# Performance work log

Hardware: AMD Instinct MI355X
Metric: run time of the kernel (lower is better)

Reference implementation:

```python
import jax, jax.numpy as jnp
import numpy as np

N_HEADS = 4
D_HEAD = 32  # out_features // n_heads = 128 // 4
NEG_SLOPE = 0.2


def setup_inputs() -> dict:
    key = jax.random.key(0)
    k_x, k_adj, k_w, k_a = jax.random.split(key, 4)
    B, N, F_in, F_out = 4, 2048, 128, 128
    x = jax.random.normal(k_x, (B, N, F_in), dtype=jnp.float32)
    adj = jax.random.randint(k_adj, (B, N, N), 0, 2, dtype=jnp.int32)
    # Linear weight stored as [in, out] (torch stores [out, in]; math identical: x @ W)
    w_scale = np.sqrt(2.0 / (F_in + F_out))  # xavier-ish
    W = jax.random.normal(k_w, (F_in, F_out), dtype=jnp.float32) * w_scale
    a = jax.random.normal(k_a, (N_HEADS, 2 * D_HEAD), dtype=jnp.float32) * np.sqrt(2.0 / (2 * D_HEAD))
    return {"x": x, "adj": adj, "W": W, "a": a}


def reference(x, adj, W, a):
    B, N, _ = x.shape
    # project and split heads: [B, H, N, D]
    h = jnp.einsum('bnf,fo->bno', x, W).reshape(B, N, N_HEADS, D_HEAD).transpose(0, 2, 1, 3)
    # additive attention logits
    e_src = jnp.einsum('bhnd,hd->bhn', h, a[:, :D_HEAD])  # [B,H,N]
    e_dst = jnp.einsum('bhnd,hd->bhn', h, a[:, D_HEAD:])  # [B,H,N]
    e = e_src[:, :, :, None] + e_dst[:, :, None, :]       # [B,H,N,N]
    e = jnp.where(e > 0, e, NEG_SLOPE * e)                # leaky_relu(0.2)
    mask = (adj[:, None, :, :] == 0)                      # [B,1,N,N] -> broadcast over heads
    e = jnp.where(mask, -jnp.inf, e)
    alpha = jax.nn.softmax(e, axis=-1)                    # dropout omitted (eval mode)
    out = jnp.einsum('bhnm,bhmd->bhnd', alpha, h)         # weighted aggregation
    out = out.transpose(0, 2, 1, 3).reshape(B, N, N_HEADS * D_HEAD)
    return jax.nn.elu(out)
```

## Files before the change

kernel.cpp:

```cpp
#include <hip/hip_runtime.h>
#include <hip/hip_bf16.h>

#define BB 4
#define NN 2048
#define FIN 128
#define NH 4
#define DH 32
#define NS 0.2f

typedef unsigned int u32;
typedef unsigned short u16;
typedef unsigned long long u64;
typedef __attribute__((ext_vector_type(8))) short short8;
typedef __attribute__((ext_vector_type(4))) float f32x4;
typedef __attribute__((ext_vector_type(4))) unsigned int u32x4;

#define OFF_ES 0
#define OFF_PQ 65536
#define OFF_HT 131088
#define OFF_BITS 655376

__device__ __forceinline__ u16 f2bf_rne(float f) {
  unsigned u = __float_as_uint(f);
  return (u16)((u + 0x7fffu + ((u >> 16) & 1u)) >> 16);
}

__device__ __forceinline__ int bitmask(u32 w, int e) {
#if __has_builtin(__builtin_amdgcn_sbfe)
  return __builtin_amdgcn_sbfe((int)w, e, 1);
#else
  return ((int)(w << (31 - e))) >> 31;
#endif
}

__global__ __launch_bounds__(256) void k_pack(const int* __restrict__ adj,
                                              u32* __restrict__ bits) {
  const int row = (blockIdx.x << 2) | (threadIdx.x >> 6);
  const int lane = threadIdx.x & 63;
  const int* src = adj + (size_t)row * NN;
  u32* dst = bits + (size_t)row * 64;
#pragma unroll 8
  for (int it = 0; it < 32; ++it) {
    const int v = src[it * 64 + lane];
    const u64 m = __ballot(v != 0);
    if (lane == 0) *(u64*)(dst + it * 2) = m;
  }
}

__global__ __launch_bounds__(256) void k_proj(
    const float* __restrict__ x, const float* __restrict__ W,
    const float* __restrict__ a, u16* __restrict__ hT,
    float* __restrict__ e_src, u32* __restrict__ PQ) {
  __shared__ float Ws[FIN * 128];
  const int tid = threadIdx.x;
  const int f = tid & 127, g = tid >> 7;
  const float4* Wg4 = (const float4*)W;
  float4* Ws4 = (float4*)Ws;
#pragma unroll
  for (int t = 0; t < 16; ++t) Ws4[t * 256 + tid] = Wg4[t * 256 + tid];
  __syncthreads();

  const int rb = blockIdx.x * 16 + g * 8;
  const int head = f >> 5, d = f & 31;
  const int b = rb >> 11, n0 = rb & (NN - 1);
  const int bh = b * NH + head;
  const float a_s = a[head * (2 * DH) + d];
  const float a_d = a[head * (2 * DH) + DH + d];

  float acc[8];
#pragma unroll
  for (int r = 0; r < 8; ++r) acc[r] = 0.f;

  const float* xb = x + (size_t)rb * FIN;
  for (int k = 0; k < FIN; ++k) {
    const float wv = Ws[k * 128 + f];
#pragma unroll
    for (int r = 0; r < 8; ++r) acc[r] = fmaf(wv, xb[r * FIN + k], acc[r]);
  }

  u16 hs[8];
#pragma unroll
  for (int r = 0; r < 8; ++r) hs[r] = f2bf_rne(acc[r]);
  u16* dst = hT + ((size_t)bh * DH + d) * NN + n0;
  *(int4*)dst = *(int4*)&hs[0];

#pragma unroll
  for (int r = 0; r < 8; ++r) {
    float s1 = acc[r] * a_s;
    float s2 = acc[r] * a_d;
#pragma unroll
    for (int off = 16; off >= 1; off >>= 1) {
      s1 += __shfl_xor(s1, off);
      s2 += __shfl_xor(s2, off);
    }
    if (d == 0) {
      e_src[(size_t)bh * NN + n0 + r] = s1;
      const u32 pb = f2bf_rne(__expf(s2));
      const u32 qb = f2bf_rne(__expf(NS * s2));
      PQ[(size_t)bh * NN + n0 + r] = (qb << 16) | pb;
    }
  }
}

__global__ __launch_bounds__(256, 4) void k_attn(
    const u16* __restrict__ hT, const float* __restrict__ e_src,
    const u32* __restrict__ PQv, const u32* __restrict__ bits,
    float* __restrict__ out) {
  __shared__ __align__(16) u16 smem[4][2][32 * 64];

  const int bid = blockIdx.x;
  const int bh = bid >> 6;
  const int it = bid & 63;
  const int b = bh >> 2, head = bh & 3;

  const int w = threadIdx.x >> 6;
  const int lane = threadIdx.x & 63;
  const int lg = lane >> 4, lm = lane & 15;

  const int i0 = it * 32 + lm;
  const int i1 = i0 + 16;
  const float es0 = e_src[(size_t)bh * NN + i0];
  const float es1 = e_src[(size_t)bh * NN + i1];
  const float A0 = __expf(es0), B0 = __expf(NS * es0);
  const float A1 = __expf(es1), B1 = __expf(NS * es1);

  const u32* PQb = PQv + (size_t)bh * NN + w * 512;
  const u16* hb = hT + (size_t)bh * DH * NN + w * 512;
  const u32* br0 = bits + ((size_t)b * NN + i0) * 64 + w * 16;
  const u32* br1 = bits + ((size_t)b * NN + i1) * 64 + w * 16;
  const int shamt = lg * 8;
  const int jb = lg * 8;

  u32 wd0[16], wd1[16];
#pragma unroll
  for (int q = 0; q < 4; ++q) {
    const u32x4 v0 = *(const u32x4*)(br0 + q * 4);
    const u32x4 v1 = *(const u32x4*)(br1 + q * 4);
#pragma unroll
    for (int k2 = 0; k2 < 4; ++k2) { wd0[q * 4 + k2] = v0[k2]; wd1[q * 4 + k2] = v1[k2]; }
  }

  const int sd = lane >> 3;
  const int sj = (lane & 7) * 8;
  u16* stg0 = &smem[w][0][0];
  u16* stg1 = &smem[w][1][0];
  const int woff = (sd * 64 + sj) ^ (sd << 3);

  short8 ones;
#pragma unroll
  for (int e = 0; e < 8; ++e) ones[e] = (short)0x3F80;

  f32x4 acc00 = {0,0,0,0}, acc01 = {0,0,0,0};
  f32x4 acc10 = {0,0,0,0}, acc11 = {0,0,0,0};
  f32x4 accS0 = {0,0,0,0}, accS1 = {0,0,0,0};

  {
    int4 r0 = *(const int4*)(hb + (size_t)(0 * 8 + sd) * NN + sj);
    int4 r1 = *(const int4*)(hb + (size_t)(1 * 8 + sd) * NN + sj);
    int4 r2 = *(const int4*)(hb + (size_t)(2 * 8 + sd) * NN + sj);
    int4 r3 = *(const int4*)(hb + (size_t)(3 * 8 + sd) * NN + sj);
    *(int4*)(stg0 + woff) = r0;
    *(int4*)(stg0 + woff + 1 * 512) = r1;
    *(int4*)(stg0 + woff + 2 * 512) = r2;
    *(int4*)(stg0 + woff + 3 * 512) = r3;
  }

  const int ra0 = (lm * 64) ^ ((lm & 7) << 3);

#pragma unroll
  for (int s = 0; s < 8; ++s) {
    u16* cur = (s & 1) ? stg1 : stg0;
    u16* nxt = (s & 1) ? stg0 : stg1;
    int4 n0, n1, n2, n3;
    if (s < 7) {
      const u16* g = hb + (s + 1) * 64;
      n0 = *(const int4*)(g + (size_t)(0 * 8 + sd) * NN + sj);
      n1 = *(const int4*)(g + (size_t)(1 * 8 + sd) * NN + sj);
      n2 = *(const int4*)(g + (size_t)(2 * 8 + sd) * NN + sj);
      n3 = *(const int4*)(g + (size_t)(3 * 8 + sd) * NN + sj);
    }
#pragma unroll
    for (int c = 0; c < 2; ++c) {
      const int jl = c * 32 + jb;
      const u32x4 pqa = *(const u32x4*)(PQb + s * 64 + jl);
      const u32x4 pqb = *(const u32x4*)(PQb + s * 64 + jl + 4);
      const short8 hv0 = *(const short8*)(cur + (ra0 ^ jl));
      const short8 hv1 = *(const short8*)(cur + ((ra0 ^ jl) + 16 * 64));
      const u32 wsh0 = wd0[s * 2 + c] >> shamt;
      const u32 wsh1 = wd1[s * 2 + c] >> shamt;
      short8 af0, af1;
#pragma unroll
      for (int e = 0; e < 8; ++e) {
        const u32 pq = (e < 4) ? pqa[e] : pqb[e - 4];
        const float Pf = __uint_as_float(pq << 16);
        const float Qf = __uint_as_float(pq & 0xffff0000u);
        const int m0 = bitmask(wsh0, e);
        const int m1 = bitmask(wsh1, e);
        float w0 = fmaxf(A0 * Pf, B0 * Qf);
        w0 = __int_as_float(__float_as_int(w0) & m0);
        af0[e] = (short)__builtin_bit_cast(unsigned short, __float2bfloat16(w0));
        float w1 = fmaxf(A1 * Pf, B1 * Qf);
        w1 = __int_as_float(__float_as_int(w1) & m1);
        af1[e] = (short)__builtin_bit_cast(unsigned short, __float2bfloat16(w1));
      }
      __builtin_amdgcn_s_setprio(1);
      acc00 = __builtin_amdgcn_mfma_f32_16x16x32_bf16(af0, hv0, acc00, 0, 0, 0);
      acc01 = __builtin_amdgcn_mfma_f32_16x16x32_bf16(af0, hv1, acc01, 0, 0, 0);
      acc10 = __builtin_amdgcn_mfma_f32_16x16x32_bf16(af1, hv0, acc10, 0, 0, 0);
      acc11 = __builtin_amdgcn_mfma_f32_16x16x32_bf16(af1, hv1, acc11, 0, 0, 0);
      accS0 = __builtin_amdgcn_mfma_f32_16x16x32_bf16(af0, ones, accS0, 0, 0, 0);
      accS1 = __builtin_amdgcn_mfma_f32_16x16x32_bf16(af1, ones, accS1, 0, 0, 0);
      __builtin_amdgcn_s_setprio(0);
    }
    if (s < 7) {
      *(int4*)(nxt + woff) = n0;
      *(int4*)(nxt + woff + 1 * 512) = n1;
      *(int4*)(nxt + woff + 2 * 512) = n2;
      *(int4*)(nxt + woff + 3 * 512) = n3;
    }
  }

  __syncthreads();
  float (*part)[32][33] = (float (*)[32][33]) & smem[0][0][0];
  float (*sp)[2][16] = (float (*)[2][16])((char*)&smem[0][0][0] + 16896);

#pragma unroll
  for (int r = 0; r < 4; ++r) {
    const int rl = lg * 4 + r;
    part[w][rl][lm] = acc00[r];
    part[w][rl][16 + lm] = acc01[r];
    part[w][16 + rl][lm] = acc10[r];
    part[w][16 + rl][16 + lm] = acc11[r];
  }
  if (lm == 0) {
#pragma unroll
    for (int r = 0; r < 4; ++r) {
      sp[w][0][lg * 4 + r] = accS0[r];
      sp[w][1][lg * 4 + r] = accS1[r];
    }
  }
  __syncthreads();

  const int tid = threadIdx.x;
#pragma unroll
  for (int t = 0; t < 4; ++t) {
    const int idx = t * 256 + tid;
    const int row = idx >> 5, d = idx & 31;
    const float v = part[0][row][d] + part[1][row][d] +
                    part[2][row][d] + part[3][row][d];
    const float s = sp[0][row >> 4][row & 15] + sp[1][row >> 4][row & 15] +
                    sp[2][row >> 4][row & 15] + sp[3][row >> 4][row & 15];
    const float o = v / s;
    const int n = it * 32 + row;
    out[((size_t)b * NN + n) * 128 + head * 32 + d] =
        o > 0.f ? o : (__expf(o) - 1.f);
  }
}

extern "C" void kernel_launch(void* const* d_in, const int* in_sizes, int n_in,
                              void* d_out, int out_size, void* d_ws, size_t ws_size,
                              hipStream_t stream) {
  const float* x = (const float*)d_in[0];
  const int* adj = (const int*)d_in[1];
  const float* W = (const float*)d_in[2];
  const float* a = (const float*)d_in[3];
  float* out = (float*)d_out;
  float* ws = (float*)d_ws;

  float* e_src = ws + OFF_ES;
  u32* PQv = (u32*)(ws + OFF_PQ);
  u16* hT = (u16*)(ws + OFF_HT);
  u32* bits = (u32*)(ws + OFF_BITS);

  k_pack<<<(BB * NN) / 4, 256, 0, stream>>>(adj, bits);
  k_proj<<<(BB * NN) / 16, 256, 0, stream>>>(x, W, a, hT, e_src, PQv);
  k_attn<<<BB * NH * 64, 256, 0, stream>>>(hT, e_src, PQv, bits, out);
}
```

Before: 62.67 us.

## Split attention key dimension across blocks and add combine kernel

Splits the neighbor (j) dimension of the attention kernel into two halves handled by separate blocks, writing unnormalized partial sums and softmax denominators to workspace, then adds a combine kernel that sums partials, normalizes and applies ELU. It also drops the LDS double-buffered staging of h and reads h fragments directly from global memory. The aim is more blocks for occupancy and shorter per-block work. In exchange it adds an extra kernel launch and round trip of partials through global memory, and uncoalesced direct global loads of h.

```diff
diff --git a/kernel.cpp b/kernel.cpp
--- a/kernel.cpp
+++ b/kernel.cpp
@@ -7,6 +7,7 @@
 #define NH 4
 #define DH 32
 #define NS 0.2f
+#define JP 2
 
 typedef unsigned int u32;
 typedef unsigned short u16;
@@ -15,10 +16,14 @@
 typedef __attribute__((ext_vector_type(4))) float f32x4;
 typedef __attribute__((ext_vector_type(4))) unsigned int u32x4;
 
-#define OFF_ES 0
-#define OFF_PQ 65536
-#define OFF_HT 131088
-#define OFF_BITS 655376
+#define OFF_ES   0
+#define OFF_PQ   32768
+#define OFF_HT   65536
+#define OFF_BITS 589824
+#define OFF_PACC 1114112
+#define OFF_PS   3211264
+#define PACC_STRIDE ((size_t)16 * NN * 32)
+#define PS_STRIDE   ((size_t)16 * NN)
 
 __device__ __forceinline__ u16 f2bf_rne(float f) {
   unsigned u = __float_as_uint(f);
@@ -102,16 +107,18 @@
   }
 }
 
-__global__ __launch_bounds__(256, 4) void k_attn(
+__global__ __launch_bounds__(256) void k_attn(
     const u16* __restrict__ hT, const float* __restrict__ e_src,
     const u32* __restrict__ PQv, const u32* __restrict__ bits,
-    float* __restrict__ out) {
-  __shared__ __align__(16) u16 smem[4][2][32 * 64];
+    float* __restrict__ pacc, float* __restrict__ pS) {
+  __shared__ float part[4][32][33];
+  __shared__ float sp[4][2][16];
 
   const int bid = blockIdx.x;
-  const int bh = bid >> 6;
+  const int jp = bid >> 10;
+  const int bh = (bid >> 6) & 15;
   const int it = bid & 63;
-  const int b = bh >> 2, head = bh & 3;
+  const int b = bh >> 2;
 
   const int w = threadIdx.x >> 6;
   const int lane = threadIdx.x & 63;
@@ -124,27 +131,24 @@
   const float A0 = __expf(es0), B0 = __expf(NS * es0);
   const float A1 = __expf(es1), B1 = __expf(NS * es1);
 
-  const u32* PQb = PQv + (size_t)bh * NN + w * 512;
-  const u16* hb = hT + (size_t)bh * DH * NN + w * 512;
-  const u32* br0 = bits + ((size_t)b * NN + i0) * 64 + w * 16;
-  const u32* br1 = bits + ((size_t)b * NN + i1) * 64 + w * 16;
+  const int jwbase = jp * 1024 + w * 256;
+  const u32* PQb = PQv + (size_t)bh * NN + jwbase;
+  const u16* hb0 = hT + ((size_t)bh * DH + lm) * NN + jwbase;
+  const u16* hb1 = hT + ((size_t)bh * DH + 16 + lm) * NN + jwbase;
+  const int wbase = jwbase >> 5;
+  const u32* br0 = bits + ((size_t)b * NN + i0) * 64 + wbase;
+  const u32* br1 = bits + ((size_t)b * NN + i1) * 64 + wbase;
   const int shamt = lg * 8;
   const int jb = lg * 8;
 
-  u32 wd0[16], wd1[16];
-#pragma unroll
-  for (int q = 0; q < 4; ++q) {
+  u32 wd0[8], wd1[8];
+#pragma unroll
+  for (int q = 0; q < 2; ++q) {
     const u32x4 v0 = *(const u32x4*)(br0 + q * 4);
     const u32x4 v1 = *(const u32x4*)(br1 + q * 4);
 #pragma unroll
     for (int k2 = 0; k2 < 4; ++k2) { wd0[q * 4 + k2] = v0[k2]; wd1[q * 4 + k2] = v1[k2]; }
   }
-
-  const int sd = lane >> 3;
-  const int sj = (lane & 7) * 8;
-  u16* stg0 = &smem[w][0][0];
-  u16* stg1 = &smem[w][1][0];
-  const int woff = (sd * 64 + sj) ^ (sd << 3);
 
   short8 ones;
 #pragma unroll
@@ -154,75 +158,39 @@
   f32x4 acc10 = {0,0,0,0}, acc11 = {0,0,0,0};
   f32x4 accS0 = {0,0,0,0}, accS1 = {0,0,0,0};
 
-  {
-    int4 r0 = *(const int4*)(hb + (size_t)(0 * 8 + sd) * NN + sj);
-    int4 r1 = *(const int4*)(hb + (size_t)(1 * 8 + sd) * NN + sj);
-    int4 r2 = *(const int4*)(hb + (size_t)(2 * 8 + sd) * NN + sj);
-    int4 r3 = *(const int4*)(hb + (size_t)(3 * 8 + sd) * NN + sj);
-    *(int4*)(stg0 + woff) = r0;
-    *(int4*)(stg0 + woff + 1 * 512) = r1;
-    *(int4*)(stg0 + woff + 2 * 512) = r2;
-    *(int4*)(stg0 + woff + 3 * 512) = r3;
-  }
-
-  const int ra0 = (lm * 64) ^ ((lm & 7) << 3);
-
-#pragma unroll
-  for (int s = 0; s < 8; ++s) {
-    u16* cur = (s & 1) ? stg1 : stg0;
-    u16* nxt = (s & 1) ? stg0 : stg1;
-    int4 n0, n1, n2, n3;
-    if (s < 7) {
-      const u16* g = hb + (s + 1) * 64;
-      n0 = *(const int4*)(g + (size_t)(0 * 8 + sd) * NN + sj);
-      n1 = *(const int4*)(g + (size_t)(1 * 8 + sd) * NN + sj);
-      n2 = *(const int4*)(g + (size_t)(2 * 8 + sd) * NN + sj);
-      n3 = *(const int4*)(g + (size_t)(3 * 8 + sd) * NN + sj);
-    }
-#pragma unroll
-    for (int c = 0; c < 2; ++c) {
-      const int jl = c * 32 + jb;
-      const u32x4 pqa = *(const u32x4*)(PQb + s * 64 + jl);
-      const u32x4 pqb = *(const u32x4*)(PQb + s * 64 + jl + 4);
-      const short8 hv0 = *(const short8*)(cur + (ra0 ^ jl));
-      const short8 hv1 = *(const short8*)(cur + ((ra0 ^ jl) + 16 * 64));
-      const u32 wsh0 = wd0[s * 2 + c] >> shamt;
-      const u32 wsh1 = wd1[s * 2 + c] >> shamt;
-      short8 af0, af1;
-#pragma unroll
-      for (int e = 0; e < 8; ++e) {
-        const u32 pq = (e < 4) ? pqa[e] : pqb[e - 4];
-        const float Pf = __uint_as_float(pq << 16);
-        const float Qf = __uint_as_float(pq & 0xffff0000u);
-        const int m0 = bitmask(wsh0, e);
-        const int m1 = bitmask(wsh1, e);
-        float w0 = fmaxf(A0 * Pf, B0 * Qf);
-        w0 = __int_as_float(__float_as_int(w0) & m0);
-        af0[e] = (short)__builtin_bit_cast(unsigned short, __float2bfloat16(w0));
-        float w1 = fmaxf(A1 * Pf, B1 * Qf);
-        w1 = __int_as_float(__float_as_int(w1) & m1);
-        af1[e] = (short)__builtin_bit_cast(unsigned short, __float2bfloat16(w1));
-      }
-      __builtin_amdgcn_s_setprio(1);
-      acc00 = __builtin_amdgcn_mfma_f32_16x16x32_bf16(af0, hv0, acc00, 0, 0, 0);
-      acc01 = __builtin_amdgcn_mfma_f32_16x16x32_bf16(af0, hv1, acc01, 0, 0, 0);
-      acc10 = __builtin_amdgcn_mfma_f32_16x16x32_bf16(af1, hv0, acc10, 0, 0, 0);
-      acc11 = __builtin_amdgcn_mfma_f32_16x16x32_bf16(af1, hv1, acc11, 0, 0, 0);
-      accS0 = __builtin_amdgcn_mfma_f32_16x16x32_bf16(af0, ones, accS0, 0, 0, 0);
-      accS1 = __builtin_amdgcn_mfma_f32_16x16x32_bf16(af1, ones, accS1, 0, 0, 0);
-      __builtin_amdgcn_s_setprio(0);
-    }
-    if (s < 7) {
-      *(int4*)(nxt + woff) = n0;
-      *(int4*)(nxt + woff + 1 * 512) = n1;
-      *(int4*)(nxt + woff + 2 * 512) = n2;
-      *(int4*)(nxt + woff + 3 * 512) = n3;
-    }
-  }
-
-  __syncthreads();
-  float (*part)[32][33] = (float (*)[32][33]) & smem[0][0][0];
-  float (*sp)[2][16] = (float (*)[2][16])((char*)&smem[0][0][0] + 16896);
+#pragma unroll
+  for (int t = 0; t < 8; ++t) {
+    const int jj = t * 32 + jb;
+    const u32x4 pqa = *(const u32x4*)(PQb + jj);
+    const u32x4 pqb = *(const u32x4*)(PQb + jj + 4);
+    const short8 hv0 = *(const short8*)(hb0 + jj);
+    const short8 hv1 = *(const short8*)(hb1 + jj);
+    const u32 wsh0 = wd0[t] >> shamt;
+    const u32 wsh1 = wd1[t] >> shamt;
+    short8 af0, af1;
+#pragma unroll
+    for (int e = 0; e < 8; ++e) {
+      const u32 pq = (e < 4) ? pqa[e] : pqb[e - 4];
+      const float Pf = __uint_as_float(pq << 16);
+      const float Qf = __uint_as_float(pq & 0xffff0000u);
+      const int m0 = bitmask(wsh0, e);
+      const int m1 = bitmask(wsh1, e);
+      float w0 = fmaxf(A0 * Pf, B0 * Qf);
+      w0 = __int_as_float(__float_as_int(w0) & m0);
+      af0[e] = (short)__builtin_bit_cast(unsigned short, __float2bfloat16(w0));
+      float w1 = fmaxf(A1 * Pf, B1 * Qf);
+      w1 = __int_as_float(__float_as_int(w1) & m1);
+      af1[e] = (short)__builtin_bit_cast(unsigned short, __float2bfloat16(w1));
+    }
+    __builtin_amdgcn_s_setprio(1);
+    acc00 = __builtin_amdgcn_mfma_f32_16x16x32_bf16(af0, hv0, acc00, 0, 0, 0);
+    acc01 = __builtin_amdgcn_mfma_f32_16x16x32_bf16(af0, hv1, acc01, 0, 0, 0);
+    acc10 = __builtin_amdgcn_mfma_f32_16x16x32_bf16(af1, hv0, acc10, 0, 0, 0);
+    acc11 = __builtin_amdgcn_mfma_f32_16x16x32_bf16(af1, hv1, acc11, 0, 0, 0);
+    accS0 = __builtin_amdgcn_mfma_f32_16x16x32_bf16(af0, ones, accS0, 0, 0, 0);
+    accS1 = __builtin_amdgcn_mfma_f32_16x16x32_bf16(af1, ones, accS1, 0, 0, 0);
+    __builtin_amdgcn_s_setprio(0);
+  }
 
 #pragma unroll
   for (int r = 0; r < 4; ++r) {
@@ -241,6 +209,8 @@
   }
   __syncthreads();
 
+  float* pa = pacc + ((size_t)jp * 16 + bh) * NN * 32;
+  float* ps = pS + ((size_t)jp * 16 + bh) * NN;
   const int tid = threadIdx.x;
 #pragma unroll
   for (int t = 0; t < 4; ++t) {
@@ -248,13 +218,34 @@
     const int row = idx >> 5, d = idx & 31;
     const float v = part[0][row][d] + part[1][row][d] +
                     part[2][row][d] + part[3][row][d];
-    const float s = sp[0][row >> 4][row & 15] + sp[1][row >> 4][row & 15] +
-                    sp[2][row >> 4][row & 15] + sp[3][row >> 4][row & 15];
-    const float o = v / s;
-    const int n = it * 32 + row;
-    out[((size_t)b * NN + n) * 128 + head * 32 + d] =
-        o > 0.f ? o : (__expf(o) - 1.f);
-  }
+    pa[(size_t)(it * 32 + row) * 32 + d] = v;
+    if (d == 0) {
+      const float s = sp[0][row >> 4][row & 15] + sp[1][row >> 4][row & 15] +
+                      sp[2][row >> 4][row & 15] + sp[3][row >> 4][row & 15];
+      ps[it * 32 + row] = s;
+    }
+  }
+}
+
+__global__ __launch_bounds__(256) void k_comb(
+    const float* __restrict__ pacc, const float* __restrict__ pS,
+    float* __restrict__ out) {
+  const int idx = blockIdx.x * 256 + threadIdx.x;
+  const int f = idx & 127;
+  const int g = idx >> 7;
+  const int b = g >> 11, n = g & (NN - 1);
+  const int head = f >> 5, d = f & 31;
+  const int bh = b * NH + head;
+  const size_t base = ((size_t)bh * NN + n) * 32 + d;
+  const size_t sbase = (size_t)bh * NN + n;
+  float v = 0.f, s = 0.f;
+#pragma unroll
+  for (int p = 0; p < JP; ++p) {
+    v += pacc[(size_t)p * PACC_STRIDE + base];
+    s += pS[(size_t)p * PS_STRIDE + sbase];
+  }
+  const float o = v / s;
+  out[idx] = o > 0.f ? o : (__expf(o) - 1.f);
 }
 
 extern "C" void kernel_launch(void* const* d_in, const int* in_sizes, int n_in,
@@ -271,8 +262,11 @@
   u32* PQv = (u32*)(ws + OFF_PQ);
   u16* hT = (u16*)(ws + OFF_HT);
   u32* bits = (u32*)(ws + OFF_BITS);
+  float* pacc = ws + OFF_PACC;
+  float* pS = ws + OFF_PS;
 
   k_pack<<<(BB * NN) / 4, 256, 0, stream>>>(adj, bits);
   k_proj<<<(BB * NN) / 16, 256, 0, stream>>>(x, W, a, hT, e_src, PQv);
-  k_attn<<<BB * NH * 64, 256, 0, stream>>>(hT, e_src, PQv, bits, out);
-}
+  k_attn<<<JP * BB * NH * 64, 256, 0, stream>>>(hT, e_src, PQv, bits, pacc, pS);
+  k_comb<<<(BB * NN * 128) / 256, 256, 0, stream>>>(pacc, pS, out);
+}
```

Measured after the change: 67.43 us. 7.6% more time.
